# Optimization experiments

Measured on AMD Instinct MI355X. Metric: run time of the kernel, lower is better.

Reference implementation:

```python
import jax, jax.numpy as jnp
import numpy as np

NEG_INF = -1e30

def setup_inputs() -> dict:
    key = jax.random.key(0)
    kx, kq, kk, kv = jax.random.split(key, 4)
    B, T, C, H = 4, 4096, 2048, 128
    x = jax.random.normal(kx, (B, T, C), dtype=jnp.float32)
    Wq = jax.random.normal(kq, (C, H), dtype=jnp.float32) * (C ** -0.5)
    Wk = jax.random.normal(kk, (C, H), dtype=jnp.float32) * (C ** -0.5)
    Wv = jax.random.normal(kv, (C, H), dtype=jnp.float32) * (C ** -0.5)
    return {"x": x, "Wq": Wq, "Wk": Wk, "Wv": Wv}

def reference(x, Wq, Wk, Wv):
    B, T, C = x.shape
    q = x @ Wq  # [B, T, H]
    k = x @ Wk
    v = x @ Wv
    # NOTE: original scales by channels**-0.5 (n_embd), not head_size**-0.5
    scale = C ** -0.5
    wei = jnp.einsum('bqh,bkh->bqk', q, k) * scale  # [B, T, T]
    causal = jnp.tril(jnp.ones((T, T), dtype=bool))
    wei = jnp.where(causal, wei, NEG_INF)
    wei = jax.nn.softmax(wei, axis=-1)
    return jnp.einsum('bqk,bkh->bqh', wei, v)
```

## Files before the change

### kernel.cpp

```cpp
#include <hip/hip_runtime.h>


typedef __attribute__((ext_vector_type(8))) short s8v;
typedef __attribute__((ext_vector_type(4))) float f4v;

__device__ __forceinline__ unsigned short f2bf(float f) {
  unsigned int b = __float_as_uint(f);
  b += 0x7FFFu + ((b >> 16) & 1u);
  return (unsigned short)(b >> 16);
}
__device__ __forceinline__ unsigned int pk2bf(float lo, float hi) {
  return (unsigned int)f2bf(lo) | ((unsigned int)f2bf(hi) << 16);
}

#define SCALE_QK 0.02209708691207961f

__global__ void prep_wt(const float* __restrict__ Wq, const float* __restrict__ Wk,
                        const float* __restrict__ Wv, unsigned short* __restrict__ WT) {
  int e = blockIdx.x * 256 + threadIdx.x;
  int m = e >> 18;
  int r = e & 262143;
  int c = r >> 7, h = r & 127;
  const float* W = (m == 0) ? Wq : (m == 1) ? Wk : Wv;
  float v = W[r];
  if (m == 0) v *= SCALE_QK;
  WT[m * 262144 + h * 2048 + c] = f2bf(v);
}

__global__ __launch_bounds__(512, 1) void proj_kernel(
    const float* __restrict__ x, const unsigned short* __restrict__ WT,
    unsigned short* __restrict__ Qo, unsigned short* __restrict__ Ko,
    unsigned short* __restrict__ VTo)
{
  __shared__ __align__(16) char psmem[116736];
  unsigned short* scr = (unsigned short*)psmem;

  const int tid = threadIdx.x;
  const int w = tid >> 6, lane = tid & 63;
  const int l15 = lane & 15, g = lane >> 4;
  const int wr = w >> 2, wc = w & 3;
  const int rowbase = blockIdx.x * 64;

  f4v acc[12];
  #pragma unroll
  for (int n = 0; n < 12; ++n) acc[n] = (f4v){0.f, 0.f, 0.f, 0.f};

  const int arow = tid >> 3;
  const int akc  = (tid & 7) * 16;
  const float* xsrc = x + (size_t)(rowbase + arow) * 2048 + (tid & 7) * 8;
  const char* WTb = (const char*)WT;

#define STAGE_B(dst_, k0_)                                                     \
  {                                                                            \
    _Pragma("unroll")                                                          \
    for (int p = 0; p < 6; ++p) {                                              \
      const int off = tid * 16 + p * 8192;                                     \
      const int row = off >> 7, chunk = off & 127;                             \
      __builtin_amdgcn_global_load_lds(                                        \
        (const __attribute__((address_space(1))) void*)(                       \
            WTb + (size_t)row * 4096 + (size_t)(k0_) * 2 +                     \
            (chunk ^ ((row & 7) << 4))),                                       \
        (__attribute__((address_space(3))) void*)((dst_) + off), 16, 0, 0);    \
    }                                                                          \
  }

#define WRITE_A(dst_, aa_, ab_)                                                \
  {                                                                            \
    s8v t_;                                                                    \
    _Pragma("unroll")                                                          \
    for (int i = 0; i < 4; ++i) { t_[i] = (short)f2bf(aa_[i]);                 \
                                  t_[i + 4] = (short)f2bf(ab_[i]); }           \
    *(s8v*)((dst_) + arow * 144 + akc) = t_;                                   \
  }

#define COMPUTE(SEL)                                                           \
  {                                                                            \
    const char* Bb = psmem + (SEL) * 49152;                                    \
    const char* Ab = psmem + 98304 + (SEL) * 9216;                             \
    s8v af[2][2], bfr[6][2];                                                   \
    _Pragma("unroll")                                                          \
    for (int mi = 0; mi < 2; ++mi)                                             \
      _Pragma("unroll")                                                        \
      for (int kk = 0; kk < 2; ++kk)                                           \
        af[mi][kk] = *(const s8v*)(Ab + (32 * wr + 16 * mi + l15) * 144 +      \
                                   kk * 64 + g * 16);                          \
    _Pragma("unroll")                                                          \
    for (int nl = 0; nl < 6; ++nl) {                                           \
      const int row = 96 * wc + 16 * nl + l15;                                 \
      _Pragma("unroll")                                                        \
      for (int kk = 0; kk < 2; ++kk)                                           \
        bfr[nl][kk] = *(const s8v*)(Bb + row * 128 +                           \
                       ((kk * 64 + g * 16) ^ ((l15 & 7) << 4)));               \
    }                                                                          \
    __builtin_amdgcn_s_setprio(1);                                             \
    _Pragma("unroll")                                                          \
    for (int kk = 0; kk < 2; ++kk)                                             \
      _Pragma("unroll")                                                        \
      for (int mi = 0; mi < 2; ++mi)                                           \
        _Pragma("unroll")                                                      \
        for (int nl = 0; nl < 6; ++nl)                                         \
          acc[mi * 6 + nl] = __builtin_amdgcn_mfma_f32_16x16x32_bf16(          \
              af[mi][kk], bfr[nl][kk], acc[mi * 6 + nl], 0, 0, 0);             \
    __builtin_amdgcn_s_setprio(0);                                             \
  }

#define PBODY(SEL, K0, XA, XB, DOX, WN)                                        \
  {                                                                            \
    if ((K0) + 64 < 2048) {                                                    \
      STAGE_B(psmem + ((SEL) ^ 1) * 49152, (K0) + 64)                          \
    }                                                                          \
    __builtin_amdgcn_sched_barrier(0);               \
    if ((K0) + 64 < 2048) {                                                    \
      WRITE_A(psmem + 98304 + ((SEL) ^ 1) * 9216, XA, XB)                      \
    }                                                                          \
    if (DOX) {                                                                 \
      XA = *(const f4v*)(xsrc + (K0) + 192);                                   \
      XB = *(const f4v*)(xsrc + (K0) + 196);                                   \
    }                                                                          \
    COMPUTE(SEL)                                                               \
    asm volatile("s_waitcnt lgkmcnt(0)" ::: "memory");                         \
    asm volatile("s_waitcnt vmcnt(" #WN ")" ::: "memory");                     \
    __builtin_amdgcn_s_barrier();                                              \
  }

  f4v xe_a = *(const f4v*)(xsrc);
  f4v xe_b = *(const f4v*)(xsrc + 4);
  STAGE_B(psmem, 0)
  __builtin_amdgcn_sched_barrier(0);
  f4v xo_a = *(const f4v*)(xsrc + 64);
  f4v xo_b = *(const f4v*)(xsrc + 68);
  WRITE_A(psmem + 98304, xe_a, xe_b)
  xe_a = *(const f4v*)(xsrc + 128);
  xe_b = *(const f4v*)(xsrc + 132);
  asm volatile("s_waitcnt lgkmcnt(0)" ::: "memory");
  asm volatile("s_waitcnt vmcnt(4)" ::: "memory");
  __builtin_amdgcn_s_barrier();

  for (int it = 0; it < 14; ++it) {
    const int k0 = it * 128;
    PBODY(0, k0, xo_a, xo_b, 1, 2)
    PBODY(1, k0 + 64, xe_a, xe_b, 1, 2)
  }
  PBODY(0, 1792, xo_a, xo_b, 1, 2)
  PBODY(1, 1856, xe_a, xe_b, 0, 0)
  PBODY(0, 1920, xo_a, xo_b, 0, 0)
  COMPUTE(1)
#undef PBODY
#undef STAGE_B
#undef WRITE_A
#undef COMPUTE

  #pragma unroll
  for (int mi = 0; mi < 2; ++mi) {
    #pragma unroll
    for (int nl = 0; nl < 6; ++nl) {
      const int colg = 96 * wc + 16 * nl + l15;
      const int m = colg >> 7;
      const int h = colg & 127;
      const f4v a = acc[mi * 6 + nl];
      if (m < 2) {
        unsigned short* dst = (m == 0) ? Qo : Ko;
        #pragma unroll
        for (int r = 0; r < 4; ++r) {
          const int t = rowbase + 32 * wr + 16 * mi + 4 * g + r;
          dst[(size_t)t * 128 + h] = f2bf(a[r]);
        }
      } else {
        #pragma unroll
        for (int r = 0; r < 4; ++r) {
          const int tl = 32 * wr + 16 * mi + 4 * g + r;
          scr[h * 72 + tl] = f2bf(a[r]);
        }
      }
    }
  }
  __syncthreads();
  {
    const int b   = rowbase >> 12;
    const int tg0 = rowbase & 4095;
    const int h    = tid >> 2;
    const int toff = (tid & 3) * 16;
    unsigned short* dst = VTo + (size_t)(b * 128 + h) * 4096 + tg0 + toff;
    *(s8v*)(dst)     = *(const s8v*)(&scr[h * 72 + toff]);
    *(s8v*)(dst + 8) = *(const s8v*)(&scr[h * 72 + toff + 8]);
  }
}

__global__ __launch_bounds__(256, 2) void attn_kernel(
    const unsigned short* __restrict__ Q, const unsigned short* __restrict__ K,
    const unsigned short* __restrict__ VT, float* __restrict__ out)
{
  __shared__ __align__(16) char smem[71168];
  unsigned short* plds = (unsigned short*)(smem + 65536);
  float* mlp = (float*)(smem + 70656);

  const int tid  = threadIdx.x;
  const int w    = tid >> 6;
  const int lane = tid & 63;
  const int l15 = lane & 15, g = lane >> 4;

  const int bid = blockIdx.x;
  const int i8  = bid & 255;
  const int j   = i8 >> 2;
  const int s   = (bid < 256) ? (127 - j) : j;
  const int b   = i8 & 3;
  const int qb = s * 32;
  const int roff = (w >> 1) * 16, half = w & 1;
  const int ntiles = (qb + 95) >> 6;

  const char* Kg = (const char*)(K  + (size_t)b * 4096 * 128);
  const char* Vg = (const char*)(VT + (size_t)b * 128 * 4096);
  const unsigned short* Qb = Q + (size_t)b * 4096 * 128;

  s8v qf[4];
  #pragma unroll
  for (int kk = 0; kk < 4; ++kk)
    qf[kk] = *(const s8v*)(Qb + (size_t)(qb + roff + l15) * 128 + kk * 32 + g * 8);

  f4v o[8];
  #pragma unroll
  for (int n = 0; n < 8; ++n) o[n] = (f4v){0.f, 0.f, 0.f, 0.f};
  float mrun = -1e30f, lrun = 0.f;

  const int off0 = tid * 16;

#define STAGE(Kl_, kvb_)                                                       \
  {                                                                            \
    char* Kl = (Kl_);                                                          \
    _Pragma("unroll")                                                          \
    for (int p = 0; p < 4; ++p) {                                              \
      const int off = off0 + p * 4096;                                         \
      const int ks = off ^ (((off >> 8) & 7) << 4);                            \
      __builtin_amdgcn_global_load_lds(                                        \
        (const __attribute__((address_space(1))) void*)(Kg + (size_t)(kvb_) * 256 + ks), \
        (__attribute__((address_space(3))) void*)(Kl + off), 16, 0, 0);        \
    }                                                                          \
    _Pragma("unroll")                                                          \
    for (int p = 0; p < 4; ++p) {                                              \
      const int off = off0 + p * 4096;                                         \
      const int h = off >> 7;                                                  \
      const int cs = (off & 127) ^ ((h & 7) << 4);                             \
      __builtin_amdgcn_global_load_lds(                                        \
        (const __attribute__((address_space(1))) void*)(Vg + (size_t)h * 8192 + (size_t)(kvb_) * 2 + cs), \
        (__attribute__((address_space(3))) void*)(Kl + 16384 + off), 16, 0, 0); \
    }                                                                          \
  }

  STAGE(smem, 0)
  __syncthreads();

  int cur = 0;
  for (int it = 0; it < ntiles; ++it) {
    const int kvb = it * 64;
    if (it + 1 < ntiles) STAGE(smem + (cur ^ 1) * 32768, kvb + 64)

    const char* Kl = smem + cur * 32768;
    const char* Vl = Kl + 16384;
    s8v kf[2][4];
    #pragma unroll
    for (int t2 = 0; t2 < 2; ++t2) {
      const int row = half * 32 + t2 * 16 + l15;
      #pragma unroll
      for (int kk = 0; kk < 4; ++kk)
        kf[t2][kk] = *(const s8v*)(Kl + ((row * 256 + kk * 64 + g * 16) ^ ((l15 & 7) << 4)));
    }
    s8v vf[8];
    #pragma unroll
    for (int n = 0; n < 8; ++n) {
      const int row = n * 16 + l15;
      vf[n] = *(const s8v*)(Vl + ((row * 128 + half * 64 + g * 16) ^ ((l15 & 7) << 4)));
    }
    f4v sc[2];
    sc[0] = (f4v){0.f, 0.f, 0.f, 0.f};
    sc[1] = (f4v){0.f, 0.f, 0.f, 0.f};
    __builtin_amdgcn_s_setprio(1);
    #pragma unroll
    for (int kk = 0; kk < 4; ++kk) {
      sc[0] = __builtin_amdgcn_mfma_f32_16x16x32_bf16(kf[0][kk], qf[kk], sc[0], 0, 0, 0);
      sc[1] = __builtin_amdgcn_mfma_f32_16x16x32_bf16(kf[1][kk], qf[kk], sc[1], 0, 0, 0);
    }
    __builtin_amdgcn_s_setprio(0);
    if (it == ntiles - 1) {
      const int qrow = qb + roff + l15;
      #pragma unroll
      for (int t2 = 0; t2 < 2; ++t2)
        #pragma unroll
        for (int r = 0; r < 4; ++r) {
          const int kv = kvb + half * 32 + 16 * t2 + 4 * g + r;
          if (kv > qrow) sc[t2][r] = -1e30f;
        }
    }
    float v = fmaxf(fmaxf(fmaxf(sc[0][0], sc[0][1]), fmaxf(sc[0][2], sc[0][3])),
                    fmaxf(fmaxf(sc[1][0], sc[1][1]), fmaxf(sc[1][2], sc[1][3])));
    v = fmaxf(v, __shfl_xor(v, 16));
    v = fmaxf(v, __shfl_xor(v, 32));
    if (__any(v > mrun + 4.0f)) {
      const float mnew = fmaxf(mrun, v);
      const float corr = __expf(mrun - mnew);
      mrun = mnew;
      lrun *= corr;
      #pragma unroll
      for (int n = 0; n < 8; ++n)
        #pragma unroll
        for (int r = 0; r < 4; ++r) o[n][r] *= corr;
    }
    f4v p0, p1;
    #pragma unroll
    for (int r = 0; r < 4; ++r) {
      p0[r] = __expf(sc[0][r] - mrun);
      p1[r] = __expf(sc[1][r] - mrun);
    }
    lrun += (p0[0] + p0[1]) + (p0[2] + p0[3]) + (p1[0] + p1[1]) + (p1[2] + p1[3]);
    unsigned short* pw = plds + w * 640;
    *(unsigned int*)(&pw[l15 * 40 + 4 * g])          = pk2bf(p0[0], p0[1]);
    *(unsigned int*)(&pw[l15 * 40 + 4 * g + 2])      = pk2bf(p0[2], p0[3]);
    *(unsigned int*)(&pw[l15 * 40 + 16 + 4 * g])     = pk2bf(p1[0], p1[1]);
    *(unsigned int*)(&pw[l15 * 40 + 16 + 4 * g + 2]) = pk2bf(p1[2], p1[3]);
    const s8v pf = *(const s8v*)(pw + l15 * 40 + g * 8);
    __builtin_amdgcn_s_setprio(1);
    #pragma unroll
    for (int n = 0; n < 8; ++n)
      o[n] = __builtin_amdgcn_mfma_f32_16x16x32_bf16(vf[n], pf, o[n], 0, 0, 0);
    __builtin_amdgcn_s_setprio(0);

    __syncthreads();
    cur ^= 1;
  }
#undef STAGE

  float lt = lrun;
  lt += __shfl_xor(lt, 16);
  lt += __shfl_xor(lt, 32);
  if (g == 0) {
    mlp[(w * 16 + l15) * 2 + 0] = mrun;
    mlp[(w * 16 + l15) * 2 + 1] = lt;
  }
  float* ol = (float*)smem;
  #pragma unroll
  for (int n = 0; n < 8; ++n)
    *(f4v*)(&ol[(w * 16 + l15) * 132 + 16 * n + 4 * g]) = o[n];
  __syncthreads();

  {
    const int st  = tid >> 7;
    const int t7  = tid & 127;
    const int row = t7 >> 3;
    const int hb  = (t7 & 7) * 16;
    const int wA = 2 * st, wB = 2 * st + 1;
    const float m0 = mlp[(wA * 16 + row) * 2], l0 = mlp[(wA * 16 + row) * 2 + 1];
    const float m1 = mlp[(wB * 16 + row) * 2], l1 = mlp[(wB * 16 + row) * 2 + 1];
    const float M  = fmaxf(m0, m1);
    const float w0 = __expf(m0 - M), w1 = __expf(m1 - M);
    const float inv = 1.0f / (w0 * l0 + w1 * l1);
    float* dst = out + (size_t)(b * 4096 + qb + 16 * st + row) * 128 + hb;
    #pragma unroll
    for (int j4 = 0; j4 < 4; ++j4) {
      const f4v a = *(const f4v*)(&ol[(wA * 16 + row) * 132 + hb + 4 * j4]);
      const f4v c = *(const f4v*)(&ol[(wB * 16 + row) * 132 + hb + 4 * j4]);
      f4v res;
      #pragma unroll
      for (int jj = 0; jj < 4; ++jj) res[jj] = (w0 * a[jj] + w1 * c[jj]) * inv;
      *(f4v*)(dst + 4 * j4) = res;
    }
  }
}

extern "C" void kernel_launch(void* const* d_in, const int* in_sizes, int n_in,
                              void* d_out, int out_size, void* d_ws, size_t ws_size,
                              hipStream_t stream) {
  const float* x  = (const float*)d_in[0];
  const float* Wq = (const float*)d_in[1];
  const float* Wk = (const float*)d_in[2];
  const float* Wv = (const float*)d_in[3];

  unsigned short* WT = (unsigned short*)d_ws;
  unsigned short* Q  = (unsigned short*)((char*)d_ws + 1572864);
  unsigned short* K  = (unsigned short*)((char*)d_ws + 5767168);
  unsigned short* VT = (unsigned short*)((char*)d_ws + 9961472);
  float* out = (float*)d_out;

  prep_wt<<<3072, 256, 0, stream>>>(Wq, Wk, Wv, WT);
  proj_kernel<<<256, 512, 0, stream>>>(x, WT, Q, K, VT);
  attn_kernel<<<512, 256, 0, stream>>>(Q, K, VT, out);
}
```

Baseline: 111.1 us.

## Double KV tile to 128 and load V fragments directly from global

Raises the KV tile from 64 to 128 keys per iteration, which halves loop iterations and barriers and gives each wave 4 score tiles and 2 PV MFMAs per output block. The LDS double buffer now holds only K. V^T fragments are read straight from global memory into registers inside the loop instead of being staged through LDS. This cuts LDS traffic and synchronization, but exposes global-load latency for V, raises register pressure, and masks more wasted work on the diagonal tile.

```diff
diff --git a/kernel.cpp b/kernel.cpp
--- a/kernel.cpp
+++ b/kernel.cpp
@@ -190,9 +190,9 @@
     const unsigned short* __restrict__ Q, const unsigned short* __restrict__ K,
     const unsigned short* __restrict__ VT, float* __restrict__ out)
 {
-  __shared__ __align__(16) char smem[71168];
+  __shared__ __align__(16) char smem[75264];
   unsigned short* plds = (unsigned short*)(smem + 65536);
-  float* mlp = (float*)(smem + 70656);
+  float* mlp = (float*)(smem + 74752);
 
   const int tid  = threadIdx.x;
   const int w    = tid >> 6;
@@ -206,10 +206,10 @@
   const int b   = i8 & 3;
   const int qb = s * 32;
   const int roff = (w >> 1) * 16, half = w & 1;
-  const int ntiles = (qb + 95) >> 6;
-
-  const char* Kg = (const char*)(K  + (size_t)b * 4096 * 128);
-  const char* Vg = (const char*)(VT + (size_t)b * 128 * 4096);
+  const int ntiles = (qb + 159) >> 7;
+
+  const char* Kg = (const char*)(K + (size_t)b * 4096 * 128);
+  const unsigned short* Vb = VT + (size_t)b * 128 * 4096;
   const unsigned short* Qb = Q + (size_t)b * 4096 * 128;
 
   s8v qf[4];
@@ -228,22 +228,13 @@
   {                                                                            \
     char* Kl = (Kl_);                                                          \
     _Pragma("unroll")                                                          \
-    for (int p = 0; p < 4; ++p) {                                              \
+    for (int p = 0; p < 8; ++p) {                                              \
       const int off = off0 + p * 4096;                                         \
       const int ks = off ^ (((off >> 8) & 7) << 4);                            \
       __builtin_amdgcn_global_load_lds(                                        \
         (const __attribute__((address_space(1))) void*)(Kg + (size_t)(kvb_) * 256 + ks), \
         (__attribute__((address_space(3))) void*)(Kl + off), 16, 0, 0);        \
     }                                                                          \
-    _Pragma("unroll")                                                          \
-    for (int p = 0; p < 4; ++p) {                                              \
-      const int off = off0 + p * 4096;                                         \
-      const int h = off >> 7;                                                  \
-      const int cs = (off & 127) ^ ((h & 7) << 4);                             \
-      __builtin_amdgcn_global_load_lds(                                        \
-        (const __attribute__((address_space(1))) void*)(Vg + (size_t)h * 8192 + (size_t)(kvb_) * 2 + cs), \
-        (__attribute__((address_space(3))) void*)(Kl + 16384 + off), 16, 0, 0); \
-    }                                                                          \
   }
 
   STAGE(smem, 0)
@@ -251,47 +242,51 @@
 
   int cur = 0;
   for (int it = 0; it < ntiles; ++it) {
-    const int kvb = it * 64;
-    if (it + 1 < ntiles) STAGE(smem + (cur ^ 1) * 32768, kvb + 64)
+    const int kvb = it * 128;
+    if (it + 1 < ntiles) STAGE(smem + (cur ^ 1) * 32768, kvb + 128)
+
+    s8v vf0[8], vf1[8];
+    #pragma unroll
+    for (int n = 0; n < 8; ++n) {
+      const unsigned short* vr = Vb + (size_t)(n * 16 + l15) * 4096
+                                 + kvb + half * 64 + g * 8;
+      vf0[n] = *(const s8v*)(vr);
+      vf1[n] = *(const s8v*)(vr + 32);
+    }
 
     const char* Kl = smem + cur * 32768;
-    const char* Vl = Kl + 16384;
-    s8v kf[2][4];
-    #pragma unroll
-    for (int t2 = 0; t2 < 2; ++t2) {
-      const int row = half * 32 + t2 * 16 + l15;
+    s8v kf[4][4];
+    #pragma unroll
+    for (int t2 = 0; t2 < 4; ++t2) {
+      const int row = half * 64 + t2 * 16 + l15;
       #pragma unroll
       for (int kk = 0; kk < 4; ++kk)
         kf[t2][kk] = *(const s8v*)(Kl + ((row * 256 + kk * 64 + g * 16) ^ ((l15 & 7) << 4)));
     }
-    s8v vf[8];
-    #pragma unroll
-    for (int n = 0; n < 8; ++n) {
-      const int row = n * 16 + l15;
-      vf[n] = *(const s8v*)(Vl + ((row * 128 + half * 64 + g * 16) ^ ((l15 & 7) << 4)));
-    }
-    f4v sc[2];
-    sc[0] = (f4v){0.f, 0.f, 0.f, 0.f};
-    sc[1] = (f4v){0.f, 0.f, 0.f, 0.f};
+    f4v sc[4];
+    #pragma unroll
+    for (int t2 = 0; t2 < 4; ++t2) sc[t2] = (f4v){0.f, 0.f, 0.f, 0.f};
     __builtin_amdgcn_s_setprio(1);
     #pragma unroll
-    for (int kk = 0; kk < 4; ++kk) {
-      sc[0] = __builtin_amdgcn_mfma_f32_16x16x32_bf16(kf[0][kk], qf[kk], sc[0], 0, 0, 0);
-      sc[1] = __builtin_amdgcn_mfma_f32_16x16x32_bf16(kf[1][kk], qf[kk], sc[1], 0, 0, 0);
-    }
+    for (int kk = 0; kk < 4; ++kk)
+      #pragma unroll
+      for (int t2 = 0; t2 < 4; ++t2)
+        sc[t2] = __builtin_amdgcn_mfma_f32_16x16x32_bf16(kf[t2][kk], qf[kk], sc[t2], 0, 0, 0);
     __builtin_amdgcn_s_setprio(0);
     if (it == ntiles - 1) {
       const int qrow = qb + roff + l15;
       #pragma unroll
-      for (int t2 = 0; t2 < 2; ++t2)
+      for (int t2 = 0; t2 < 4; ++t2)
         #pragma unroll
         for (int r = 0; r < 4; ++r) {
-          const int kv = kvb + half * 32 + 16 * t2 + 4 * g + r;
+          const int kv = kvb + half * 64 + 16 * t2 + 4 * g + r;
           if (kv > qrow) sc[t2][r] = -1e30f;
         }
     }
     float v = fmaxf(fmaxf(fmaxf(sc[0][0], sc[0][1]), fmaxf(sc[0][2], sc[0][3])),
                     fmaxf(fmaxf(sc[1][0], sc[1][1]), fmaxf(sc[1][2], sc[1][3])));
+    v = fmaxf(v, fmaxf(fmaxf(fmaxf(sc[2][0], sc[2][1]), fmaxf(sc[2][2], sc[2][3])),
+                       fmaxf(fmaxf(sc[3][0], sc[3][1]), fmaxf(sc[3][2], sc[3][3]))));
     v = fmaxf(v, __shfl_xor(v, 16));
     v = fmaxf(v, __shfl_xor(v, 32));
     if (__any(v > mrun + 4.0f)) {
@@ -304,23 +299,29 @@
         #pragma unroll
         for (int r = 0; r < 4; ++r) o[n][r] *= corr;
     }
-    f4v p0, p1;
-    #pragma unroll
-    for (int r = 0; r < 4; ++r) {
-      p0[r] = __expf(sc[0][r] - mrun);
-      p1[r] = __expf(sc[1][r] - mrun);
-    }
-    lrun += (p0[0] + p0[1]) + (p0[2] + p0[3]) + (p1[0] + p1[1]) + (p1[2] + p1[3]);
-    unsigned short* pw = plds + w * 640;
-    *(unsigned int*)(&pw[l15 * 40 + 4 * g])          = pk2bf(p0[0], p0[1]);
-    *(unsigned int*)(&pw[l15 * 40 + 4 * g + 2])      = pk2bf(p0[2], p0[3]);
-    *(unsigned int*)(&pw[l15 * 40 + 16 + 4 * g])     = pk2bf(p1[0], p1[1]);
-    *(unsigned int*)(&pw[l15 * 40 + 16 + 4 * g + 2]) = pk2bf(p1[2], p1[3]);
-    const s8v pf = *(const s8v*)(pw + l15 * 40 + g * 8);
+    f4v p[4];
+    #pragma unroll
+    for (int t2 = 0; t2 < 4; ++t2)
+      #pragma unroll
+      for (int r = 0; r < 4; ++r)
+        p[t2][r] = __expf(sc[t2][r] - mrun);
+    #pragma unroll
+    for (int t2 = 0; t2 < 4; ++t2)
+      lrun += (p[t2][0] + p[t2][1]) + (p[t2][2] + p[t2][3]);
+    unsigned short* pw = plds + w * 1152;
+    #pragma unroll
+    for (int t2 = 0; t2 < 4; ++t2) {
+      *(unsigned int*)(&pw[l15 * 72 + 16 * t2 + 4 * g])     = pk2bf(p[t2][0], p[t2][1]);
+      *(unsigned int*)(&pw[l15 * 72 + 16 * t2 + 4 * g + 2]) = pk2bf(p[t2][2], p[t2][3]);
+    }
+    const s8v pf0 = *(const s8v*)(pw + l15 * 72 + g * 8);
+    const s8v pf1 = *(const s8v*)(pw + l15 * 72 + 32 + g * 8);
     __builtin_amdgcn_s_setprio(1);
     #pragma unroll
-    for (int n = 0; n < 8; ++n)
-      o[n] = __builtin_amdgcn_mfma_f32_16x16x32_bf16(vf[n], pf, o[n], 0, 0, 0);
+    for (int n = 0; n < 8; ++n) {
+      o[n] = __builtin_amdgcn_mfma_f32_16x16x32_bf16(vf0[n], pf0, o[n], 0, 0, 0);
+      o[n] = __builtin_amdgcn_mfma_f32_16x16x32_bf16(vf1[n], pf1, o[n], 0, 0, 0);
+    }
     __builtin_amdgcn_s_setprio(0);
 
     __syncthreads();
```

New measurement: 136.6 us. +23.0%, slower.
